# Kernel optimization log

Measured on AMD Instinct MI355X. Metric: run time of the kernel, lower is better.

Reference implementation:

```python
import jax, jax.numpy as jnp
import numpy as np

B, LP, LQ, H = 32, 2048, 512, 1024

def setup_inputs() -> dict:
    key = jax.random.key(0)
    k1, k2, k3, k4 = jax.random.split(key, 4)
    p_encode = jax.random.normal(k1, (B, LP, H), dtype=jnp.float32)
    q_encode = jax.random.normal(k2, (B, LQ, H), dtype=jnp.float32)
    # nn.Linear(H, H): weight [out, in], bias [out]
    bound = 1.0 / np.sqrt(H)
    G_weight = jax.random.uniform(k3, (H, H), dtype=jnp.float32, minval=-bound, maxval=bound)
    G_bias = jax.random.uniform(k4, (H,), dtype=jnp.float32, minval=-bound, maxval=bound)
    return {"p_encode": p_encode, "q_encode": q_encode, "G_weight": G_weight, "G_bias": G_bias}

def reference(p_encode, q_encode, G_weight, G_bias):
    # q_project = transpose(G(q_encode), -2, -1): [B, H, LQ]
    q_proj = jnp.einsum('bqh,oh->bqo', q_encode, G_weight) + G_bias  # [B, LQ, H]
    # att_matrix = bmm(p_encode, q_project^T): [B, LP, LQ]
    att = jnp.einsum('bph,bqh->bpq', p_encode, q_proj)
    # m_p = softmax over LQ (dim=-1) @ q_encode -> [B, LP, H]
    m_p = jnp.einsum('bpq,bqh->bph', jax.nn.softmax(att, axis=-1), q_encode)
    # m_q = softmax over LP (dim=-2), transposed, @ p_encode -> [B, LQ, H]
    m_q = jnp.einsum('bpq,bph->bqh', jax.nn.softmax(att, axis=-2), p_encode)
    return (m_p, m_q)
```

## Files before the change

### kernel.cpp

```cpp
#include <hip/hip_runtime.h>

typedef _Float16 half_t;
typedef _Float16 f16x8 __attribute__((ext_vector_type(8)));
typedef _Float16 f16x4 __attribute__((ext_vector_type(4)));
typedef float    f32x4 __attribute__((ext_vector_type(4)));
typedef float    f32x16 __attribute__((ext_vector_type(16)));

typedef const __attribute__((address_space(1))) void cg_void;
typedef __attribute__((address_space(3))) void lds_void;

#define BB 32
#define LP 2048
#define LQ 512
#define HH 1024

enum { M_QPROJ = 0, M_OUT32 = 1 };

__global__ void cvt16_k(const float* __restrict__ w, half_t* __restrict__ o) {
  long i = ((long)blockIdx.x * 256 + threadIdx.x) * 4;
  f32x4 v = *(const f32x4*)(w + i);
  f16x4 h;
  h[0] = (half_t)v[0]; h[1] = (half_t)v[1]; h[2] = (half_t)v[2]; h[3] = (half_t)v[3];
  *(f16x4*)(o + i) = h;
}

__global__ __launch_bounds__(256) void dualcvt_k(const float* __restrict__ in,
                                                 half_t* __restrict__ rm,
                                                 half_t* __restrict__ tr,
                                                 int R, int C) {
  __shared__ half_t tile[64 * 64];
  const long zb = blockIdx.z;
  const float* src = in + zb * (long)R * C;
  half_t* dstT = tr + zb * (long)C * R;
  half_t* dstR = rm + zb * (long)R * C;
  const int r0 = blockIdx.y * 64, c0 = blockIdx.x * 64;
  const int t = threadIdx.x;
  const int cl = (t & 15) * 4;
  const int rl = t >> 4;
#pragma unroll
  for (int rr = 0; rr < 4; rr++) {
    int r = rr * 16 + rl;
    f32x4 v = *(const f32x4*)(src + (long)(r0 + r) * C + c0 + cl);
    f16x4 h;
#pragma unroll
    for (int j = 0; j < 4; j++) {
      h[j] = (half_t)v[j];
      int c = cl + j;
      tile[c * 64 + (r ^ (((c >> 3) & 7) << 3))] = h[j];
    }
    *(f16x4*)(dstR + (long)(r0 + r) * C + c0 + cl) = h;
  }
  __syncthreads();
  const int c = t >> 2;
  const int rch = (t & 3) * 16;
  const int m = (c >> 3) & 7;
  const int B0 = c * 64 + (rch ^ ((m << 3) & 48));
  const int hi = (m & 1) << 3;
  f16x8 g0 = *(const f16x8*)&tile[B0 + hi];
  f16x8 g1 = *(const f16x8*)&tile[B0 + (8 ^ hi)];
  half_t* dp = dstT + (long)(c0 + c) * R + r0 + rch;
  *(f16x8*)dp = g0;
  *(f16x8*)(dp + 8) = g1;
}

__global__ __launch_bounds__(256) void cfin_k(const float* __restrict__ pmg,
                                              const float* __restrict__ psg,
                                              float* __restrict__ cmax,
                                              float* __restrict__ cinv) {
  long i = (long)blockIdx.x * 256 + threadIdx.x;
  long b = i / LQ, q = i - b * LQ;
  const float* mp = pmg + (b * 16) * LQ + q;
  const float* sp = psg + (b * 16) * LQ + q;
  float m = -3e38f, s = 0.f;
#pragma unroll
  for (int t = 0; t < 16; t++) {
    float mm = mp[(long)t * LQ], ss = sp[(long)t * LQ];
    float nm = fmaxf(m, mm);
    s = s * __expf(m - nm) + ss * __expf(mm - nm);
    m = nm;
  }
  cmax[i] = m;
  cinv[i] = 1.f / s;
}

__global__ __launch_bounds__(256) void pq_k(const half_t* __restrict__ E,
                                            half_t* __restrict__ out,
                                            const float* __restrict__ pmg,
                                            const float* __restrict__ cmax,
                                            const float* __restrict__ cinv) {
  __shared__ half_t tile[64 * 64];
  const long zb = blockIdx.z;
  const half_t* src = E + zb * (long)LP * LQ;
  half_t* dst = out + zb * (long)LQ * LP;
  const int r0 = blockIdx.y * 64, c0 = blockIdx.x * 64;
  const int tIdx = r0 >> 7;
  const int t = threadIdx.x;
  const int cl = (t & 15) * 4;
  const int rl = t >> 4;
  f32x4 tm = *(const f32x4*)(pmg + ((long)zb * 16 + tIdx) * LQ + c0 + cl);
  f32x4 cm = *(const f32x4*)(cmax + (long)zb * LQ + c0 + cl);
  f32x4 ci = *(const f32x4*)(cinv + (long)zb * LQ + c0 + cl);
  float sc[4];
#pragma unroll
  for (int j = 0; j < 4; j++) sc[j] = __expf(tm[j] - cm[j]) * ci[j];
#pragma unroll
  for (int rr = 0; rr < 4; rr++) {
    int r = rr * 16 + rl;
    f16x4 v = *(const f16x4*)(src + (long)(r0 + r) * LQ + c0 + cl);
#pragma unroll
    for (int j = 0; j < 4; j++) {
      float x = (float)v[j] * sc[j];
      int c = cl + j;
      tile[c * 64 + (r ^ (((c >> 3) & 7) << 3))] = (half_t)x;
    }
  }
  __syncthreads();
  const int c = t >> 2;
  const int rch = (t & 3) * 16;
  const int m = (c >> 3) & 7;
  const int B0 = c * 64 + (rch ^ ((m << 3) & 48));
  const int hi = (m & 1) << 3;
  f16x8 g0 = *(const f16x8*)&tile[B0 + hi];
  f16x8 g1 = *(const f16x8*)&tile[B0 + (8 ^ hi)];
  half_t* dp = dst + (long)(c0 + c) * LP + r0 + rch;
  *(f16x8*)dp = g0;
  *(f16x8*)(dp + 8) = g1;
}

template<int ROWS>
__device__ __forceinline__ void stage_op(const half_t* src, int ld,
                                         half_t* lds_base, int wid, int lane) {
  const int goff = (((lane & 3) ^ ((lane >> 3) & 3)) << 3);
#pragma unroll
  for (int j = 0; j < ROWS / 128; ++j) {
    int row = j * 128 + wid * 16 + (lane >> 2);
    const half_t* g = src + (long)row * ld + goff;
    __builtin_amdgcn_global_load_lds((cg_void*)g,
        (lds_void*)(lds_base + j * 4096 + wid * 512), 16, 0, 0);
  }
}

__device__ __forceinline__ void xcd_swz(long lid, long nwg, long& out) {
  const long q8 = nwg >> 3, r8 = nwg & 7;
  const long xcd = lid & 7, rest = lid >> 3;
  out = (xcd < r8 ? xcd * (q8 + 1) : r8 * (q8 + 1) + (xcd - r8) * q8) + rest;
}

__global__ __launch_bounds__(512, 2) void attf_k(
    const half_t* __restrict__ Ap,
    const half_t* __restrict__ Bp,
    half_t* __restrict__ PpO,
    half_t* __restrict__ EO,
    float* __restrict__ pmg, float* __restrict__ psg) {
  __shared__ __align__(16) half_t As[3 * 4096];
  __shared__ __align__(16) half_t Bs[3 * 16384];
  __shared__ float rmL[4][128];
  __shared__ float cmL[2][512];
  __shared__ float rsL[4][128];
  __shared__ float csL[2][512];

  const int nby = gridDim.y;
  long lid;
  xcd_swz(blockIdx.y + (long)nby * blockIdx.z, (long)nby * gridDim.z, lid);
  const int by = (int)(lid % nby);
  const int bz = (int)(lid / nby);

  const int t0 = threadIdx.x;
  const int lane = t0 & 63;
  const int wid = t0 >> 6;
  const int wm = wid >> 2, wn = wid & 3;
  const int m0 = by * 128;

  const half_t* Abase = Ap + ((long)bz * LP + m0) * HH;
  const half_t* Bbase = Bp + (long)bz * LQ * HH;

  const int c5 = lane & 31, hi = lane >> 5;
  const int sx = (c5 >> 1) & 3;
  const int ofs0 = c5 * 32 + ((hi ^ sx) << 3);
  const int ofs1 = c5 * 32 + (((2 | hi) ^ sx) << 3);

  f32x16 acc[2][4] = {};
  const int NT = HH / 32;

#pragma unroll
  for (int tt = 0; tt < 2; ++tt) {
    stage_op<128>(Abase + tt * 32, HH, As + tt * 4096, wid, lane);
    stage_op<512>(Bbase + tt * 32, HH, Bs + tt * 16384, wid, lane);
  }

  for (int t = 0; t < NT; ++t) {
    if (t + 1 < NT) asm volatile("s_waitcnt vmcnt(5)" ::: "memory");
    else            asm volatile("s_waitcnt vmcnt(0)" ::: "memory");
    __builtin_amdgcn_s_barrier();
    asm volatile("" ::: "memory");

    const half_t* Au = As + (t % 3) * 4096;
    const half_t* Bu = Bs + (t % 3) * 16384;
    f16x8 af[2][2], bf[4][2];
#pragma unroll
    for (int mf = 0; mf < 2; ++mf) {
      const half_t* p = Au + (wm * 64 + mf * 32) * 32;
      af[mf][0] = *(const f16x8*)(p + ofs0);
      af[mf][1] = *(const f16x8*)(p + ofs1);
    }
#pragma unroll
    for (int nf = 0; nf < 4; ++nf) {
      const half_t* p = Bu + (wn * 128 + nf * 32) * 32;
      bf[nf][0] = *(const f16x8*)(p + ofs0);
      bf[nf][1] = *(const f16x8*)(p + ofs1);
    }
    if (t + 2 < NT) {
      const int u2 = (t + 2) % 3;
      stage_op<128>(Abase + (t + 2) * 32, HH, As + u2 * 4096, wid, lane);
      stage_op<512>(Bbase + (t + 2) * 32, HH, Bs + u2 * 16384, wid, lane);
    }
    __builtin_amdgcn_s_setprio(1);
#pragma unroll
    for (int mf = 0; mf < 2; ++mf)
#pragma unroll
      for (int nf = 0; nf < 4; ++nf) {
        acc[mf][nf] = __builtin_amdgcn_mfma_f32_32x32x16_f16(af[mf][0], bf[nf][0], acc[mf][nf], 0, 0, 0);
        acc[mf][nf] = __builtin_amdgcn_mfma_f32_32x32x16_f16(af[mf][1], bf[nf][1], acc[mf][nf], 0, 0, 0);
      }
    __builtin_amdgcn_s_setprio(0);
  }

  float rmv[2][16], cmv[4];
#pragma unroll
  for (int m = 0; m < 2; ++m)
#pragma unroll
    for (int r = 0; r < 16; ++r) {
      float v = fmaxf(fmaxf(acc[m][0][r], acc[m][1][r]), fmaxf(acc[m][2][r], acc[m][3][r]));
#pragma unroll
      for (int o = 1; o < 32; o <<= 1) v = fmaxf(v, __shfl_xor(v, o, 64));
      rmv[m][r] = v;
    }
#pragma unroll
  for (int n = 0; n < 4; ++n) {
    float v = acc[0][n][0];
#pragma unroll
    for (int m = 0; m < 2; ++m)
#pragma unroll
      for (int r = 0; r < 16; ++r) v = fmaxf(v, acc[m][n][r]);
    v = fmaxf(v, __shfl_xor(v, 32, 64));
    cmv[n] = v;
  }
  if (c5 < 16) {
#pragma unroll
    for (int m = 0; m < 2; ++m)
      rmL[wn][wm * 64 + m * 32 + (c5 & 3) + 8 * (c5 >> 2) + 4 * hi] = rmv[m][c5];
  }
  if (hi == 0) {
#pragma unroll
    for (int n = 0; n < 4; ++n) cmL[wm][wn * 128 + n * 32 + c5] = cmv[n];
  }
  __syncthreads();
  if (t0 < 128)
    rmL[0][t0] = fmaxf(fmaxf(rmL[0][t0], rmL[1][t0]), fmaxf(rmL[2][t0], rmL[3][t0]));
  {
    float cm2 = fmaxf(cmL[0][t0 & 511], cmL[1][t0 & 511]);
    cmL[0][t0 & 511] = cm2;
    pmg[((long)bz * 16 + by) * LQ + (t0 & 511)] = cm2;
  }
  __syncthreads();
#pragma unroll
  for (int m = 0; m < 2; ++m)
#pragma unroll
    for (int r = 0; r < 16; ++r)
      rmv[m][r] = rmL[0][wm * 64 + m * 32 + (r & 3) + 8 * (r >> 2) + 4 * hi];
#pragma unroll
  for (int n = 0; n < 4; ++n) cmv[n] = cmL[0][wn * 128 + n * 32 + c5];

  half_t* EB = EO + (long)bz * LP * LQ;
  half_t* PpB = PpO + (long)bz * LP * LQ;
  float rwS[2][16];
  float csW[4] = {0.f, 0.f, 0.f, 0.f};
#pragma unroll
  for (int m = 0; m < 2; ++m)
#pragma unroll
    for (int r = 0; r < 16; ++r) {
      long grow = (long)(m0 + wm * 64 + m * 32 + (r & 3) + 8 * (r >> 2) + 4 * hi) * LQ;
      float s = 0.f;
#pragma unroll
      for (int n = 0; n < 4; ++n) {
        float a = acc[m][n][r];
        float e = __expf(a - cmv[n]);
        csW[n] += e;
        EB[grow + wn * 128 + n * 32 + c5] = (half_t)e;
        float p = __expf(a - rmv[m][r]);
        acc[m][n][r] = p;
        s += p;
      }
#pragma unroll
      for (int o = 1; o < 32; o <<= 1) s += __shfl_xor(s, o, 64);
      rwS[m][r] = s;
    }
#pragma unroll
  for (int n = 0; n < 4; ++n) csW[n] += __shfl_xor(csW[n], 32, 64);
  if (c5 < 16) {
#pragma unroll
    for (int m = 0; m < 2; ++m)
      rsL[wn][wm * 64 + m * 32 + (c5 & 3) + 8 * (c5 >> 2) + 4 * hi] = rwS[m][c5];
  }
  if (hi == 0) {
#pragma unroll
    for (int n = 0; n < 4; ++n) csL[wm][wn * 128 + n * 32 + c5] = csW[n];
  }
  __syncthreads();
  if (t0 < 128)
    rsL[0][t0] = 1.f / (rsL[0][t0] + rsL[1][t0] + rsL[2][t0] + rsL[3][t0]);
  psg[((long)bz * 16 + by) * LQ + (t0 & 511)] = csL[0][t0 & 511] + csL[1][t0 & 511];
  __syncthreads();
#pragma unroll
  for (int m = 0; m < 2; ++m)
#pragma unroll
    for (int r = 0; r < 16; ++r) {
      long grow = (long)(m0 + wm * 64 + m * 32 + (r & 3) + 8 * (r >> 2) + 4 * hi) * LQ;
      float ri = rsL[0][wm * 64 + m * 32 + (r & 3) + 8 * (r >> 2) + 4 * hi];
#pragma unroll
      for (int n = 0; n < 4; ++n)
        PpB[grow + wn * 128 + n * 32 + c5] = (half_t)(acc[m][n][r] * ri);
    }
}

template<int MODE, int BM>
__global__ __launch_bounds__(512, 2) void gemm_k(
    const half_t* __restrict__ Ap, const half_t* __restrict__ Bp, void* __restrict__ Cp,
    const float* __restrict__ bias,
    int lda, int ldb, int ldc, int K,
    long sA, long sB, long sC) {
  constexpr int NMF = BM / 64;
  constexpr int AS = BM * 32;
  __shared__ __align__(16) half_t As[4 * AS];
  __shared__ __align__(16) half_t Bs[4 * 8192];

  const int nbx = gridDim.x, nby = gridDim.y;
  long lid;
  xcd_swz(blockIdx.x + (long)nbx * (blockIdx.y + (long)nby * blockIdx.z),
          (long)nbx * nby * gridDim.z, lid);
  const int bx = (int)(lid % nbx);
  const long tmp = lid / nbx;
  const int by = (int)(tmp % nby);
  const int bz = (int)(tmp / nby);

  const int t0 = threadIdx.x;
  const int lane = t0 & 63;
  const int wid = t0 >> 6;
  const int wm = wid >> 2, wn = wid & 3;
  const int m0 = by * BM, n0 = bx * 256;

  const half_t* Abase = Ap + sA * bz + (long)m0 * lda;
  const half_t* Bbase = Bp + sB * bz + (long)n0 * ldb;

  const int c5 = lane & 31, hi = lane >> 5;
  const int sx = (c5 >> 1) & 3;
  const int ofs0 = c5 * 32 + ((hi ^ sx) << 3);
  const int ofs1 = c5 * 32 + (((2 | hi) ^ sx) << 3);

  f32x16 acc[NMF][2] = {};
  const int NT = K >> 5;

#pragma unroll
  for (int tt = 0; tt < 3; ++tt) {
    stage_op<BM>(Abase + tt * 32, lda, As + tt * AS, wid, lane);
    stage_op<256>(Bbase + tt * 32, ldb, Bs + tt * 8192, wid, lane);
  }

  for (int t = 0; t < NT; ++t) {
    if (t + 2 < NT) {
      if constexpr (BM == 256) asm volatile("s_waitcnt vmcnt(8)" ::: "memory");
      else                     asm volatile("s_waitcnt vmcnt(6)" ::: "memory");
    } else if (t + 1 < NT) {
      if constexpr (BM == 256) asm volatile("s_waitcnt vmcnt(4)" ::: "memory");
      else                     asm volatile("s_waitcnt vmcnt(3)" ::: "memory");
    } else {
      asm volatile("s_waitcnt vmcnt(0)" ::: "memory");
    }
    __builtin_amdgcn_s_barrier();
    asm volatile("" ::: "memory");

    const half_t* Au = As + (t & 3) * AS;
    const half_t* Bu = Bs + (t & 3) * 8192;
    f16x8 af[NMF][2], bf[2][2];
#pragma unroll
    for (int mf = 0; mf < NMF; ++mf) {
      const half_t* p = Au + (wm * (BM / 2) + mf * 32) * 32;
      af[mf][0] = *(const f16x8*)(p + ofs0);
      af[mf][1] = *(const f16x8*)(p + ofs1);
    }
#pragma unroll
    for (int nf = 0; nf < 2; ++nf) {
      const half_t* p = Bu + (wn * 64 + nf * 32) * 32;
      bf[nf][0] = *(const f16x8*)(p + ofs0);
      bf[nf][1] = *(const f16x8*)(p + ofs1);
    }
    if (t + 3 < NT) {
      const int u3 = (t + 3) & 3;
      stage_op<BM>(Abase + (t + 3) * 32, lda, As + u3 * AS, wid, lane);
      stage_op<256>(Bbase + (t + 3) * 32, ldb, Bs + u3 * 8192, wid, lane);
    }
    __builtin_amdgcn_s_setprio(1);
#pragma unroll
    for (int mf = 0; mf < NMF; ++mf)
#pragma unroll
      for (int nf = 0; nf < 2; ++nf) {
        acc[mf][nf] = __builtin_amdgcn_mfma_f32_32x32x16_f16(af[mf][0], bf[nf][0], acc[mf][nf], 0, 0, 0);
        acc[mf][nf] = __builtin_amdgcn_mfma_f32_32x32x16_f16(af[mf][1], bf[nf][1], acc[mf][nf], 0, 0, 0);
      }
    __builtin_amdgcn_s_setprio(0);
  }

#pragma unroll
  for (int nf = 0; nf < 2; ++nf) {
    int col = n0 + wn * 64 + nf * 32 + c5;
    float bv = 0.f;
    if constexpr (MODE == M_QPROJ) bv = bias[col];
#pragma unroll
    for (int mf = 0; mf < NMF; ++mf) {
      int rbase = m0 + wm * (BM / 2) + mf * 32 + 4 * hi;
#pragma unroll
      for (int r = 0; r < 16; ++r) {
        int row = rbase + (r & 3) + 8 * (r >> 2);
        if constexpr (MODE == M_QPROJ)
          ((half_t*)Cp)[(long)row * ldc + col] = (half_t)(acc[mf][nf][r] + bv);
        else
          ((float*)Cp)[sC * bz + (long)row * ldc + col] = acc[mf][nf][r];
      }
    }
  }
}

extern "C" void kernel_launch(void* const* d_in, const int* in_sizes, int n_in,
                              void* d_out, int out_size, void* d_ws, size_t ws_size,
                              hipStream_t stream) {
  const float* p_enc = (const float*)d_in[0];
  const float* q_enc = (const float*)d_in[1];
  const float* Gw    = (const float*)d_in[2];
  const float* Gb    = (const float*)d_in[3];
  float* m_p = (float*)d_out;
  float* m_q = m_p + (long)BB * LP * HH;

  half_t* w16   = (half_t*)d_ws;
  half_t* q16   = w16 + (long)HH * HH;
  half_t* qT16  = q16 + (long)BB * LQ * HH;
  half_t* qpj16 = qT16 + (long)BB * HH * LQ;
  half_t* p16   = qpj16 + (long)BB * LQ * HH;
  half_t* pT16  = p16 + (long)BB * LP * HH;
  half_t* Pp    = pT16 + (long)BB * HH * LP;
  half_t* Ebuf  = Pp + (long)BB * LP * LQ;
  half_t* Pq    = Ebuf + (long)BB * LP * LQ;
  float*  cmaxb = (float*)(Pq + (long)BB * LQ * LP);
  float*  cinvb = cmaxb + (long)BB * LQ;
  float*  pmg   = cinvb + (long)BB * LQ;
  float*  psg   = pmg + (long)BB * 16 * LQ;

  cvt16_k<<<HH * HH / 1024, 256, 0, stream>>>(Gw, w16);

  dualcvt_k<<<dim3(HH / 64, LQ / 64, BB), 256, 0, stream>>>(q_enc, q16, qT16, LQ, HH);

  gemm_k<M_QPROJ, 256><<<dim3(HH / 256, BB * LQ / 256, 1), 512, 0, stream>>>(
      q16, w16, qpj16, Gb, HH, HH, HH, HH, 0, 0, 0);

  dualcvt_k<<<dim3(HH / 64, LP / 64, BB), 256, 0, stream>>>(p_enc, p16, pT16, LP, HH);

  attf_k<<<dim3(1, LP / 128, BB), 512, 0, stream>>>(p16, qpj16, Pp, Ebuf, pmg, psg);

  cfin_k<<<BB * LQ / 256, 256, 0, stream>>>(pmg, psg, cmaxb, cinvb);
  pq_k<<<dim3(LQ / 64, LP / 64, BB), 256, 0, stream>>>(Ebuf, Pq, pmg, cmaxb, cinvb);

  gemm_k<M_OUT32, 256><<<dim3(HH / 256, LP / 256, BB), 512, 0, stream>>>(
      Pp, qT16, m_p, nullptr, LQ, LQ, HH, LQ,
      (long)LP * LQ, (long)HH * LQ, (long)LP * HH);

  gemm_k<M_OUT32, 128><<<dim3(HH / 256, LQ / 128, BB), 512, 0, stream>>>(
      Pq, pT16, m_q, nullptr, LP, LP, HH, LP,
      (long)LQ * LP, (long)HH * LP, (long)LQ * HH);
}
```

Baseline: 585.4 us.

## Fuse column-softmax scaling into m_q GEMM and write E transposed from attention kernel

The attention kernel now writes the column-exponential tile E already transposed, staging it through LDS, and packs exp values as fp16 pairs in the accumulator registers. The separate pq_k pass, which read E, rescaled it and transposed it into Pq, is removed. A small stf_k kernel computes per-tile column scale factors, and a new mqf_k GEMM applies them while staging the A operand. This removes one full read/write pass over a 32x2048x512 fp16 buffer. In exchange the attention epilogue gains extra LDS transposes and barriers, and the scale is applied in fp16.

```diff
diff --git a/kernel.cpp b/kernel.cpp
--- a/kernel.cpp
+++ b/kernel.cpp
@@ -63,68 +63,27 @@
   *(f16x8*)(dp + 8) = g1;
 }
 
-__global__ __launch_bounds__(256) void cfin_k(const float* __restrict__ pmg,
-                                              const float* __restrict__ psg,
-                                              float* __restrict__ cmax,
-                                              float* __restrict__ cinv) {
+__global__ __launch_bounds__(256) void stf_k(const float* __restrict__ pmg,
+                                             const float* __restrict__ psg,
+                                             half_t* __restrict__ stf) {
   long i = (long)blockIdx.x * 256 + threadIdx.x;
-  long b = i / LQ, q = i - b * LQ;
+  long b = i >> 9, q = i & 511;
   const float* mp = pmg + (b * 16) * LQ + q;
   const float* sp = psg + (b * 16) * LQ + q;
+  float mv[16];
   float m = -3e38f, s = 0.f;
 #pragma unroll
   for (int t = 0; t < 16; t++) {
-    float mm = mp[(long)t * LQ], ss = sp[(long)t * LQ];
+    float mm = mp[(long)t * LQ]; mv[t] = mm;
+    float ss = sp[(long)t * LQ];
     float nm = fmaxf(m, mm);
     s = s * __expf(m - nm) + ss * __expf(mm - nm);
     m = nm;
   }
-  cmax[i] = m;
-  cinv[i] = 1.f / s;
-}
-
-__global__ __launch_bounds__(256) void pq_k(const half_t* __restrict__ E,
-                                            half_t* __restrict__ out,
-                                            const float* __restrict__ pmg,
-                                            const float* __restrict__ cmax,
-                                            const float* __restrict__ cinv) {
-  __shared__ half_t tile[64 * 64];
-  const long zb = blockIdx.z;
-  const half_t* src = E + zb * (long)LP * LQ;
-  half_t* dst = out + zb * (long)LQ * LP;
-  const int r0 = blockIdx.y * 64, c0 = blockIdx.x * 64;
-  const int tIdx = r0 >> 7;
-  const int t = threadIdx.x;
-  const int cl = (t & 15) * 4;
-  const int rl = t >> 4;
-  f32x4 tm = *(const f32x4*)(pmg + ((long)zb * 16 + tIdx) * LQ + c0 + cl);
-  f32x4 cm = *(const f32x4*)(cmax + (long)zb * LQ + c0 + cl);
-  f32x4 ci = *(const f32x4*)(cinv + (long)zb * LQ + c0 + cl);
-  float sc[4];
-#pragma unroll
-  for (int j = 0; j < 4; j++) sc[j] = __expf(tm[j] - cm[j]) * ci[j];
-#pragma unroll
-  for (int rr = 0; rr < 4; rr++) {
-    int r = rr * 16 + rl;
-    f16x4 v = *(const f16x4*)(src + (long)(r0 + r) * LQ + c0 + cl);
-#pragma unroll
-    for (int j = 0; j < 4; j++) {
-      float x = (float)v[j] * sc[j];
-      int c = cl + j;
-      tile[c * 64 + (r ^ (((c >> 3) & 7) << 3))] = (half_t)x;
-    }
-  }
-  __syncthreads();
-  const int c = t >> 2;
-  const int rch = (t & 3) * 16;
-  const int m = (c >> 3) & 7;
-  const int B0 = c * 64 + (rch ^ ((m << 3) & 48));
-  const int hi = (m & 1) << 3;
-  f16x8 g0 = *(const f16x8*)&tile[B0 + hi];
-  f16x8 g1 = *(const f16x8*)&tile[B0 + (8 ^ hi)];
-  half_t* dp = dst + (long)(c0 + c) * LP + r0 + rch;
-  *(f16x8*)dp = g0;
-  *(f16x8*)(dp + 8) = g1;
+  float inv = 1.f / s;
+#pragma unroll
+  for (int t = 0; t < 16; t++)
+    stf[(b * 16 + t) * LQ + q] = (half_t)(__expf(mv[t] - m) * inv);
 }
 
 template<int ROWS>
@@ -146,11 +105,18 @@
   out = (xcd < r8 ? xcd * (q8 + 1) : r8 * (q8 + 1) + (xcd - r8) * q8) + rest;
 }
 
+__device__ __forceinline__ f16x8 sc8(f16x8 v, half_t s) {
+  f16x8 r;
+#pragma unroll
+  for (int j = 0; j < 8; ++j) r[j] = v[j] * s;
+  return r;
+}
+
 __global__ __launch_bounds__(512, 2) void attf_k(
     const half_t* __restrict__ Ap,
     const half_t* __restrict__ Bp,
     half_t* __restrict__ PpO,
-    half_t* __restrict__ EO,
+    half_t* __restrict__ Et,
     float* __restrict__ pmg, float* __restrict__ psg) {
   __shared__ __align__(16) half_t As[3 * 4096];
   __shared__ __align__(16) half_t Bs[3 * 16384];
@@ -271,36 +237,50 @@
 #pragma unroll
   for (int n = 0; n < 4; ++n) cmv[n] = cmL[0][wn * 128 + n * 32 + c5];
 
-  half_t* EB = EO + (long)bz * LP * LQ;
-  half_t* PpB = PpO + (long)bz * LP * LQ;
-  float rwS[2][16];
+  float rowS[2][16];
+#pragma unroll
+  for (int m = 0; m < 2; ++m)
+#pragma unroll
+    for (int r = 0; r < 16; ++r) rowS[m][r] = 0.f;
   float csW[4] = {0.f, 0.f, 0.f, 0.f};
 #pragma unroll
   for (int m = 0; m < 2; ++m)
 #pragma unroll
+    for (int n = 0; n < 4; ++n) {
+      float tp[16], te[16];
+#pragma unroll
+      for (int r = 0; r < 16; ++r) {
+        float a = acc[m][n][r];
+        float p = __expf(a - rmv[m][r]);
+        float e = __expf(a - cmv[n]);
+        rowS[m][r] += p;
+        csW[n] += e;
+        tp[r] = p; te[r] = e;
+      }
+#pragma unroll
+      for (int j = 0; j < 8; ++j) {
+        union { _Float16 h[2]; float f; } up, ue;
+        up.h[0] = (half_t)tp[2 * j]; up.h[1] = (half_t)tp[2 * j + 1];
+        ue.h[0] = (half_t)te[2 * j]; ue.h[1] = (half_t)te[2 * j + 1];
+        acc[m][n][j] = up.f;
+        acc[m][n][8 + j] = ue.f;
+      }
+    }
+#pragma unroll
+  for (int m = 0; m < 2; ++m)
+#pragma unroll
     for (int r = 0; r < 16; ++r) {
-      long grow = (long)(m0 + wm * 64 + m * 32 + (r & 3) + 8 * (r >> 2) + 4 * hi) * LQ;
-      float s = 0.f;
-#pragma unroll
-      for (int n = 0; n < 4; ++n) {
-        float a = acc[m][n][r];
-        float e = __expf(a - cmv[n]);
-        csW[n] += e;
-        EB[grow + wn * 128 + n * 32 + c5] = (half_t)e;
-        float p = __expf(a - rmv[m][r]);
-        acc[m][n][r] = p;
-        s += p;
-      }
+      float s = rowS[m][r];
 #pragma unroll
       for (int o = 1; o < 32; o <<= 1) s += __shfl_xor(s, o, 64);
-      rwS[m][r] = s;
+      rowS[m][r] = s;
     }
 #pragma unroll
   for (int n = 0; n < 4; ++n) csW[n] += __shfl_xor(csW[n], 32, 64);
   if (c5 < 16) {
 #pragma unroll
     for (int m = 0; m < 2; ++m)
-      rsL[wn][wm * 64 + m * 32 + (c5 & 3) + 8 * (c5 >> 2) + 4 * hi] = rwS[m][c5];
+      rsL[wn][wm * 64 + m * 32 + (c5 & 3) + 8 * (c5 >> 2) + 4 * hi] = rowS[m][c5];
   }
   if (hi == 0) {
 #pragma unroll
@@ -311,16 +291,57 @@
     rsL[0][t0] = 1.f / (rsL[0][t0] + rsL[1][t0] + rsL[2][t0] + rsL[3][t0]);
   psg[((long)bz * 16 + by) * LQ + (t0 & 511)] = csL[0][t0 & 511] + csL[1][t0 & 511];
   __syncthreads();
+
+  half_t* PpB = PpO + (long)bz * LP * LQ;
 #pragma unroll
   for (int m = 0; m < 2; ++m)
 #pragma unroll
-    for (int r = 0; r < 16; ++r) {
-      long grow = (long)(m0 + wm * 64 + m * 32 + (r & 3) + 8 * (r >> 2) + 4 * hi) * LQ;
-      float ri = rsL[0][wm * 64 + m * 32 + (r & 3) + 8 * (r >> 2) + 4 * hi];
-#pragma unroll
-      for (int n = 0; n < 4; ++n)
-        PpB[grow + wn * 128 + n * 32 + c5] = (half_t)(acc[m][n][r] * ri);
-    }
+    for (int j = 0; j < 8; ++j) {
+      int r0a = 2 * j, r1a = 2 * j + 1;
+      int row0 = wm * 64 + m * 32 + (r0a & 3) + 8 * (r0a >> 2) + 4 * hi;
+      int row1 = wm * 64 + m * 32 + (r1a & 3) + 8 * (r1a >> 2) + 4 * hi;
+      float ri0 = rsL[0][row0], ri1 = rsL[0][row1];
+#pragma unroll
+      for (int n = 0; n < 4; ++n) {
+        union { _Float16 h[2]; float f; } u; u.f = acc[m][n][j];
+        int col = wn * 128 + n * 32 + c5;
+        PpB[(long)(m0 + row0) * LQ + col] = (half_t)((float)u.h[0] * ri0);
+        PpB[(long)(m0 + row1) * LQ + col] = (half_t)((float)u.h[1] * ri1);
+      }
+    }
+
+  half_t* TQ = Bs;
+  half_t* EtB = Et + (long)bz * LQ * LP;
+#pragma unroll
+  for (int rr2 = 0; rr2 < 4; ++rr2) {
+    __syncthreads();
+    if (wn == rr2) {
+#pragma unroll
+      for (int m = 0; m < 2; ++m)
+#pragma unroll
+        for (int n = 0; n < 4; ++n)
+#pragma unroll
+          for (int g = 0; g < 4; ++g) {
+            int q_l = n * 32 + c5;
+            int pblk = wm * 8 + m * 4 + g;
+            int ah = q_l * 128 + ((pblk ^ (q_l & 7)) << 3) + 4 * hi;
+            union { float f[2]; f16x4 h4; } u;
+            u.f[0] = acc[m][n][8 + 2 * g];
+            u.f[1] = acc[m][n][8 + 2 * g + 1];
+            *(f16x4*)&TQ[ah] = u.h4;
+          }
+    }
+    __syncthreads();
+    {
+      int q_l = t0 >> 2;
+#pragma unroll
+      for (int i2 = 0; i2 < 4; ++i2) {
+        int pc = (t0 & 3) + 4 * i2;
+        f16x8 v = *(const f16x8*)&TQ[q_l * 128 + ((pc ^ (q_l & 7)) << 3)];
+        *(f16x8*)&EtB[(long)(rr2 * 128 + q_l) * LP + m0 + pc * 8] = v;
+      }
+    }
+  }
 }
 
 template<int MODE, int BM>
@@ -430,6 +451,119 @@
   }
 }
 
+__global__ __launch_bounds__(512, 2) void mqf_k(
+    const half_t* __restrict__ Et,
+    const half_t* __restrict__ Bp,
+    const half_t* __restrict__ stf,
+    float* __restrict__ Cp) {
+  __shared__ __align__(16) half_t Asb[2][128 * 32];
+  __shared__ __align__(16) half_t Bsb[3][256 * 32];
+  __shared__ half_t scL[16 * 128];
+
+  const int nbx = gridDim.x, nby = gridDim.y;
+  long lid;
+  xcd_swz(blockIdx.x + (long)nbx * (blockIdx.y + (long)nby * blockIdx.z),
+          (long)nbx * nby * gridDim.z, lid);
+  const int bx = (int)(lid % nbx);
+  const long tmp = lid / nbx;
+  const int by = (int)(tmp % nby);
+  const int bz = (int)(tmp / nby);
+
+  const int t0 = threadIdx.x;
+  const int lane = t0 & 63;
+  const int wid = t0 >> 6;
+  const int wm = wid >> 2, wn = wid & 3;
+  const int q0 = by * 128, n0 = bx * 256;
+
+  const half_t* Abase = Et + ((long)bz * LQ + q0) * LP;
+  const half_t* Bbase = Bp + ((long)bz * HH + n0) * LP;
+
+  if (t0 < 256) {
+    f16x8 v = *(const f16x8*)(stf + ((long)bz * 16 + (t0 >> 4)) * LQ + q0 + (t0 & 15) * 8);
+    *(f16x8*)&scL[(t0 >> 4) * 128 + (t0 & 15) * 8] = v;
+  }
+  __syncthreads();
+
+  const int arow = t0 >> 2, aslot = t0 & 3;
+  const int awoff = arow * 32 + ((aslot ^ ((arow >> 1) & 3)) << 3);
+  const half_t* agp = Abase + (long)arow * LP + aslot * 8;
+
+  const int c5 = lane & 31, hi = lane >> 5;
+  const int sx = (c5 >> 1) & 3;
+  const int ofs0 = c5 * 32 + ((hi ^ sx) << 3);
+  const int ofs1 = c5 * 32 + (((2 | hi) ^ sx) << 3);
+
+  f32x16 acc[2][2] = {};
+  const int NT = LP / 32;
+
+  stage_op<256>(Bbase + 0, LP, Bsb[0], wid, lane);
+  stage_op<256>(Bbase + 32, LP, Bsb[1], wid, lane);
+  f16x8 aA = *(const f16x8*)(agp + 0);
+  f16x8 aB = *(const f16x8*)(agp + 32);
+  *(f16x8*)&Asb[0][awoff] = sc8(aA, scL[arow]);
+  asm volatile("s_waitcnt vmcnt(2)" ::: "memory");
+
+#define MQ_BODY(T, CURBUF, NXTBUF, USEREG, LOADREG)                            \
+  {                                                                            \
+    const int t = (T);                                                         \
+    if (t + 1 < NT) asm volatile("s_waitcnt vmcnt(3) lgkmcnt(0)" ::: "memory");\
+    else            asm volatile("s_waitcnt vmcnt(0) lgkmcnt(0)" ::: "memory");\
+    __builtin_amdgcn_s_barrier();                                              \
+    asm volatile("" ::: "memory");                                             \
+    if (t + 2 < NT) {                                                          \
+      stage_op<256>(Bbase + (t + 2) * 32, LP, Bsb[(t + 2) % 3], wid, lane);    \
+      LOADREG = *(const f16x8*)(agp + (t + 2) * 32);                           \
+    }                                                                          \
+    const half_t* Au = Asb[CURBUF];                                            \
+    const half_t* Bu = Bsb[t % 3];                                             \
+    f16x8 af[2][2], bf[2][2];                                                  \
+    _Pragma("unroll")                                                          \
+    for (int mf = 0; mf < 2; ++mf) {                                           \
+      const half_t* p = Au + (wm * 64 + mf * 32) * 32;                         \
+      af[mf][0] = *(const f16x8*)(p + ofs0);                                   \
+      af[mf][1] = *(const f16x8*)(p + ofs1);                                   \
+    }                                                                          \
+    _Pragma("unroll")                                                          \
+    for (int nf = 0; nf < 2; ++nf) {                                           \
+      const half_t* p = Bu + (wn * 64 + nf * 32) * 32;                         \
+      bf[nf][0] = *(const f16x8*)(p + ofs0);                                   \
+      bf[nf][1] = *(const f16x8*)(p + ofs1);                                   \
+    }                                                                          \
+    if (t + 1 < NT)                                                            \
+      *(f16x8*)&Asb[NXTBUF][awoff] =                                           \
+          sc8(USEREG, scL[((t + 1) >> 2) * 128 + arow]);                       \
+    __builtin_amdgcn_s_setprio(1);                                             \
+    _Pragma("unroll")                                                          \
+    for (int mf = 0; mf < 2; ++mf)                                             \
+      _Pragma("unroll")                                                        \
+      for (int nf = 0; nf < 2; ++nf) {                                         \
+        acc[mf][nf] = __builtin_amdgcn_mfma_f32_32x32x16_f16(af[mf][0], bf[nf][0], acc[mf][nf], 0, 0, 0); \
+        acc[mf][nf] = __builtin_amdgcn_mfma_f32_32x32x16_f16(af[mf][1], bf[nf][1], acc[mf][nf], 0, 0, 0); \
+      }                                                                        \
+    __builtin_amdgcn_s_setprio(0);                                             \
+  }
+
+  for (int tt = 0; tt < NT; tt += 2) {
+    MQ_BODY(tt,     0, 1, aB, aA)
+    MQ_BODY(tt + 1, 1, 0, aA, aB)
+  }
+#undef MQ_BODY
+
+#pragma unroll
+  for (int nf = 0; nf < 2; ++nf) {
+    int col = n0 + wn * 64 + nf * 32 + c5;
+#pragma unroll
+    for (int mf = 0; mf < 2; ++mf) {
+      int rbase = q0 + wm * 64 + mf * 32 + 4 * hi;
+#pragma unroll
+      for (int r = 0; r < 16; ++r) {
+        int row = rbase + (r & 3) + 8 * (r >> 2);
+        Cp[(long)bz * LQ * HH + (long)row * HH + col] = acc[mf][nf][r];
+      }
+    }
+  }
+}
+
 extern "C" void kernel_launch(void* const* d_in, const int* in_sizes, int n_in,
                               void* d_out, int out_size, void* d_ws, size_t ws_size,
                               hipStream_t stream) {
@@ -447,11 +581,9 @@
   half_t* p16   = qpj16 + (long)BB * LQ * HH;
   half_t* pT16  = p16 + (long)BB * LP * HH;
   half_t* Pp    = pT16 + (long)BB * HH * LP;
-  half_t* Ebuf  = Pp + (long)BB * LP * LQ;
-  half_t* Pq    = Ebuf + (long)BB * LP * LQ;
-  float*  cmaxb = (float*)(Pq + (long)BB * LQ * LP);
-  float*  cinvb = cmaxb + (long)BB * LQ;
-  float*  pmg   = cinvb + (long)BB * LQ;
+  half_t* Et    = Pp + (long)BB * LP * LQ;
+  half_t* stfb  = Et + (long)BB * LQ * LP;
+  float*  pmg   = (float*)(stfb + (long)BB * 16 * LQ);
   float*  psg   = pmg + (long)BB * 16 * LQ;
 
   cvt16_k<<<HH * HH / 1024, 256, 0, stream>>>(Gw, w16);
@@ -463,16 +595,13 @@
 
   dualcvt_k<<<dim3(HH / 64, LP / 64, BB), 256, 0, stream>>>(p_enc, p16, pT16, LP, HH);
 
-  attf_k<<<dim3(1, LP / 128, BB), 512, 0, stream>>>(p16, qpj16, Pp, Ebuf, pmg, psg);
-
-  cfin_k<<<BB * LQ / 256, 256, 0, stream>>>(pmg, psg, cmaxb, cinvb);
-  pq_k<<<dim3(LQ / 64, LP / 64, BB), 256, 0, stream>>>(Ebuf, Pq, pmg, cmaxb, cinvb);
+  attf_k<<<dim3(1, LP / 128, BB), 512, 0, stream>>>(p16, qpj16, Pp, Et, pmg, psg);
+
+  stf_k<<<BB * LQ / 256, 256, 0, stream>>>(pmg, psg, stfb);
 
   gemm_k<M_OUT32, 256><<<dim3(HH / 256, LP / 256, BB), 512, 0, stream>>>(
       Pp, qT16, m_p, nullptr, LQ, LQ, HH, LQ,
       (long)LP * LQ, (long)HH * LQ, (long)LP * HH);
 
-  gemm_k<M_OUT32, 128><<<dim3(HH / 256, LQ / 128, BB), 512, 0, stream>>>(
-      Pq, pT16, m_q, nullptr, LP, LP, HH, LP,
-      (long)LQ * LP, (long)HH * LP, (long)LQ * HH);
-}
+  mqf_k<<<dim3(HH / 256, LQ / 128, BB), 512, 0, stream>>>(Et, pT16, stfb, m_q);
+}
```

Measured after the change: 668.9 us. 14.3% more time.
